# Performance work log

Measured on AMD Instinct MI355X. Metric: run time of the kernel, lower is better.

## Reference

```python
import jax, jax.numpy as jnp
import numpy as np

D_MODEL = 1024  # scaling uses sqrt(d_model), as in the source


def setup_inputs() -> dict:
    key = jax.random.key(0)
    kx, kq, kk, kv = jax.random.split(key, 4)
    B, N, D, H = 4, 4096, D_MODEL, 128
    X = jax.random.normal(kx, (B, N, D), dtype=jnp.float32)
    # nn.Linear(d_model, d_head, bias=False) weights, stored as [d_model, d_head]
    s = 1.0 / np.sqrt(D)
    Wq = jax.random.normal(kq, (D, H), dtype=jnp.float32) * s
    Wk = jax.random.normal(kk, (D, H), dtype=jnp.float32) * s
    Wv = jax.random.normal(kv, (D, H), dtype=jnp.float32) * s
    return {"X": X, "Wq": Wq, "Wk": Wk, "Wv": Wv}


def reference(X, Wq, Wk, Wv):
    # Q, K, V: [B, N, H]
    Q = jnp.einsum("bnd,dh->bnh", X, Wq)
    K = jnp.einsum("bnd,dh->bnh", X, Wk)
    V = jnp.einsum("bnd,dh->bnh", X, Wv)
    # Scores: [B, N, N]; source divides by sqrt(d_model) (not sqrt(d_head))
    A = jnp.einsum("bqh,bkh->bqk", Q, K) / jnp.sqrt(jnp.float32(D_MODEL))
    A = jax.nn.softmax(A, axis=-1)
    # Dropout is identity in eval mode (deterministic reference baseline)
    return jnp.einsum("bqk,bkh->bqh", A, V)
```

## Files before the change

### kernel.cpp

```cpp
#include <hip/hip_runtime.h>
#include <stdint.h>

typedef __bf16 bf16_t;
typedef bf16_t bf16x8 __attribute__((ext_vector_type(8)));
typedef float f32x4 __attribute__((ext_vector_type(4)));
typedef float f32x16 __attribute__((ext_vector_type(16)));
typedef unsigned short u16;
typedef unsigned int u32;

#define MFMA16(a, b, c) __builtin_amdgcn_mfma_f32_16x16x32_bf16((a), (b), (c), 0, 0, 0)
#define MFMA32(a, b, c) __builtin_amdgcn_mfma_f32_32x32x16_bf16((a), (b), (c), 0, 0, 0)

#define QSCALE 0.04508422002778633f

__device__ __forceinline__ u16 f2bf(float f) {
  union { float f; unsigned u; } v; v.f = f;
  unsigned r = v.u + 0x7fffu + ((v.u >> 16) & 1u);
  return (u16)(r >> 16);
}

__device__ __forceinline__ float exp2x(float x) {
#if __has_builtin(__builtin_amdgcn_exp2f)
  return __builtin_amdgcn_exp2f(x);
#else
  return exp2f(x);
#endif
}

__device__ __forceinline__ float rcpx(float x) {
#if __has_builtin(__builtin_amdgcn_rcpf)
  return __builtin_amdgcn_rcpf(x);
#else
  return 1.0f / x;
#endif
}

__device__ __forceinline__ void async_cp16(const void* g, void* l) {
  __builtin_amdgcn_global_load_lds(
      (__attribute__((address_space(1))) void*)(void*)g,
      (__attribute__((address_space(3))) void*)l, 16, 0, 0);
}

__device__ __forceinline__ u32 cvtpk(float lo, float hi) {
  u32 r;
  asm("v_cvt_pk_bf16_f32 %0, %1, %2" : "=v"(r) : "v"(lo), "v"(hi));
  return r;
}
__device__ __forceinline__ void pl32swap(u32& a, u32& b) {
  asm volatile("v_permlane32_swap_b32 %0, %1" : "+v"(a), "+v"(b));
}

__global__ __launch_bounds__(256) void pack_w_k(const float* __restrict__ Wq,
                                                const float* __restrict__ Wk,
                                                const float* __restrict__ Wv,
                                                u16* __restrict__ wp) {
  int t = blockIdx.x * 256 + threadIdx.x;
  int mat = t >> 14;
  int rr = t & 16383;
  int frag = rr >> 6, lane = rr & 63;
  int nt = frag >> 5, kc = frag & 31;
  const float* W = (mat == 0) ? Wq : ((mat == 1) ? Wk : Wv);
  int k0 = kc * 32 + ((lane >> 4) << 3);
  int col = nt * 16 + (lane & 15);
  union { u16 h[8]; uint4 q; } u_;
#pragma unroll
  for (int j = 0; j < 8; ++j) u_.h[j] = f2bf(W[(size_t)(k0 + j) * 128 + col]);
  *(uint4*)(wp + (size_t)t * 8) = u_.q;
}

__device__ __forceinline__ void qkv_stage(const char* Xb, char* dst, int m0,
                                          int kc, int tid) {
#pragma unroll
  for (int i = 0; i < 2; ++i) {
    int p = i * 4096 + tid * 16;
    int row = p >> 8, cb = p & 255;
    int ucb = cb ^ ((row & 7) << 4);
    async_cp16(Xb + ((size_t)(m0 + row) * 4096 + (size_t)kc * 256 + ucb),
               dst + p);
  }
}

__global__ __launch_bounds__(256) void qkv_k(const float* __restrict__ X,
                                             const u16* __restrict__ wp,
                                             u16* __restrict__ Qb,
                                             u16* __restrict__ Kb,
                                             u16* __restrict__ Vt) {
  __shared__ __align__(16) char xs[2][8192];
  const int tid = threadIdx.x;
  const int w = tid >> 6, lane = tid & 63;
  const int r16 = lane >> 4, c16 = lane & 15;
  const int m0 = blockIdx.x * 32;
  const char* Xb = (const char*)X;

  f32x4 acc[2][6];
#pragma unroll
  for (int mt = 0; mt < 2; ++mt)
#pragma unroll
    for (int i = 0; i < 6; ++i) acc[mt][i] = (f32x4){0.f, 0.f, 0.f, 0.f};

  qkv_stage(Xb, xs[0], m0, 0, tid);
  qkv_stage(Xb, xs[1], m0, 1, tid);

  for (int kc = 0; kc < 16; ++kc) {
    if (kc + 1 < 16) {
      asm volatile("s_waitcnt vmcnt(2)" ::: "memory");
    } else {
      asm volatile("s_waitcnt vmcnt(0)" ::: "memory");
    }
    __builtin_amdgcn_s_barrier();
    asm volatile("" ::: "memory");

    const char* xb = xs[kc & 1];
    bf16x8 bw[6][2];
#pragma unroll
    for (int i = 0; i < 6; ++i) {
      int t = w + 4 * i;
      int mat = t >> 3, nt = t & 7;
      const u16* bp = wp + (size_t)mat * 131072 +
                      (size_t)((nt * 32 + kc * 2) * 64 + lane) * 8;
      bw[i][0] = *(const bf16x8*)(bp);
      bw[i][1] = *(const bf16x8*)(bp + 512);
    }
    bf16x8 a[2][2];
#pragma unroll
    for (int mt = 0; mt < 2; ++mt)
#pragma unroll
      for (int ks = 0; ks < 2; ++ks) {
        int row = mt * 16 + c16;
        int swz = (row & 7) << 4;
        int cb0 = ks * 128 + r16 * 32;
        f32x4 lo = *(const f32x4*)(xb + row * 256 + (cb0 ^ swz));
        f32x4 hi = *(const f32x4*)(xb + row * 256 + ((cb0 + 16) ^ swz));
        union { u32 u[4]; bf16x8 v; } pu;
        pu.u[0] = cvtpk(lo[0], lo[1]);
        pu.u[1] = cvtpk(lo[2], lo[3]);
        pu.u[2] = cvtpk(hi[0], hi[1]);
        pu.u[3] = cvtpk(hi[2], hi[3]);
        a[mt][ks] = pu.v;
      }
#pragma unroll
    for (int i = 0; i < 6; ++i)
#pragma unroll
      for (int ks = 0; ks < 2; ++ks)
#pragma unroll
        for (int mt = 0; mt < 2; ++mt)
          acc[mt][i] = MFMA16(a[mt][ks], bw[i][ks], acc[mt][i]);

    asm volatile("" ::: "memory");
    __builtin_amdgcn_s_barrier();
    asm volatile("" ::: "memory");
    if (kc + 2 < 16) qkv_stage(Xb, xs[kc & 1], m0, kc + 2, tid);
  }

  const int batch = m0 >> 12;
#pragma unroll
  for (int i = 0; i < 6; ++i) {
    int t = w + 4 * i;
    int mat = t >> 3, nt = t & 7;
#pragma unroll
    for (int mt = 0; mt < 2; ++mt) {
      f32x4 v = acc[mt][i];
      if (mat == 2) {
        int d = nt * 16 + c16;
        int nloc = (m0 & 4095) + mt * 16 + r16 * 4;
        union { u16 h[4]; uint2 q; } u_;
#pragma unroll
        for (int r = 0; r < 4; ++r) u_.h[r] = f2bf(v[r]);
        *(uint2*)(Vt + ((size_t)(batch * 128 + d)) * 4096 + nloc) = u_.q;
      } else {
        u16* dstm = (mat == 0) ? Qb : Kb;
        float sc = (mat == 0) ? QSCALE : 1.0f;
#pragma unroll
        for (int r = 0; r < 4; ++r) {
          int row = m0 + mt * 16 + r16 * 4 + r;
          dstm[(size_t)row * 128 + nt * 16 + c16] = f2bf(v[r] * sc);
        }
      }
    }
  }
}

__global__ __launch_bounds__(256) void pack_kv_k(const u16* __restrict__ Kb,
                                                 const u16* __restrict__ Vt,
                                                 u16* __restrict__ Kf,
                                                 u16* __restrict__ Vf) {
  int t = blockIdx.x * 256 + threadIdx.x;
  int lane = t & 63, l31 = lane & 31, hi = (lane >> 5) & 1;
  if (t < 262144) {
    int frag = t >> 6;
    int batch = frag >> 10, kt = (frag >> 3) & 127, kc = frag & 7;
    const u16* src = Kb + ((size_t)batch * 4096 + kt * 32 + l31) * 128 + kc * 16 + hi * 8;
    *(uint4*)(Kf + (size_t)t * 8) = *(const uint4*)src;
  } else {
    int o = t - 262144;
    int frag = o >> 6;
    int batch = frag >> 10, tt = (frag >> 4) & 63, ks = (frag >> 2) & 3, dt = frag & 3;
    const u16* src = Vt + ((size_t)batch * 128 + dt * 32 + l31) * 4096 + tt * 64 + ks * 16 + hi * 8;
    *(uint4*)(Vf + (size_t)o * 8) = *(const uint4*)src;
  }
}

__device__ __forceinline__ void stage16(const char* src, char* dst, int tid) {
#pragma unroll
  for (int i = 0; i < 4; ++i)
    async_cp16(src + i * 4096 + tid * 16, dst + i * 4096 + tid * 16);
}

__global__ __launch_bounds__(256, 3) void attn_k(const u16* __restrict__ Qb,
                                                 const u16* __restrict__ Kf,
                                                 const u16* __restrict__ Vf,
                                                 _Float16* __restrict__ Opart,
                                                 float* __restrict__ Ml,
                                                 int nsplit) {
  __shared__ __align__(16) char smem[49152];
  const int tid = threadIdx.x;
  const int w = tid >> 6, lane = tid & 63;
  const int l31 = lane & 31, hi = lane >> 5;

  const int B = gridDim.x;
  int xcd = blockIdx.x & 7, idx = blockIdx.x >> 3;
  int linear = xcd * (B >> 3) + idx;
  int qt = linear & 31, g = linear >> 5;
  int batch = g / nsplit, split = g - batch * nsplit;
  const int q0 = qt * 128;
  const int t0 = (split * 64) / nsplit;
  const int t1 = ((split + 1) * 64) / nsplit;
  const int T = t1 - t0;

  const char* kfc = (const char*)Kf + (size_t)batch * 1048576 + (size_t)t0 * 16384;
  const char* vfc = (const char*)Vf + (size_t)batch * 1048576 + (size_t)t0 * 16384;
  char* vbuf = smem + 32768;

  bf16x8 qf[8];
  const u16* qrow = Qb + ((size_t)batch * 4096 + q0 + w * 32 + l31) * 128 + hi * 8;
#pragma unroll
  for (int kc = 0; kc < 8; ++kc) qf[kc] = *(const bf16x8*)(qrow + kc * 16);

  f32x16 acc[4];
#pragma unroll
  for (int dt = 0; dt < 4; ++dt)
#pragma unroll
    for (int j = 0; j < 16; ++j) acc[dt][j] = 0.f;
  float lacc[8];
#pragma unroll
  for (int i = 0; i < 8; ++i) lacc[i] = 0.f;

  stage16(kfc, smem, tid);
  stage16(vfc, vbuf, tid);
  if (T > 1) stage16(kfc + 16384, smem + 16384, tid);

  for (int t = 0; t < T; ++t) {
    if (t + 1 < T) {
      asm volatile("s_waitcnt vmcnt(8)" ::: "memory");
    } else {
      asm volatile("s_waitcnt vmcnt(4)" ::: "memory");
    }
    __builtin_amdgcn_s_barrier();
    asm volatile("" ::: "memory");
    const char* kb = smem + (t & 1) * 16384;

    f32x16 sv[2];
    __builtin_amdgcn_s_setprio(1);
#pragma unroll
    for (int nt = 0; nt < 2; ++nt) {
      f32x16 s = {};
#pragma unroll
      for (int kc = 0; kc < 8; ++kc) {
        bf16x8 kf = *(const bf16x8*)(kb + (nt * 8 + kc) * 1024 + lane * 16);
        s = MFMA32(kf, qf[kc], s);
      }
      sv[nt] = s;
    }
    __builtin_amdgcn_s_setprio(0);

#pragma unroll
    for (int nt = 0; nt < 2; ++nt)
#pragma unroll
      for (int i = 0; i < 16; ++i) sv[nt][i] = exp2x(sv[nt][i]);
#pragma unroll
    for (int i = 0; i < 8; ++i)
      lacc[i] += (sv[0][i] + sv[0][i + 8]) + (sv[1][i] + sv[1][i + 8]);

    bf16x8 pf[4];
#pragma unroll
    for (int nt = 0; nt < 2; ++nt)
#pragma unroll
      for (int half = 0; half < 2; ++half) {
        const float* p = (const float*)&sv[nt] + half * 8;
        u32 a0 = cvtpk(p[0], p[1]);
        u32 b0 = cvtpk(p[4], p[5]);
        u32 c0 = cvtpk(p[2], p[3]);
        u32 d0 = cvtpk(p[6], p[7]);
        pl32swap(a0, b0);
        pl32swap(c0, d0);
        union { u32 u[4]; bf16x8 v; } pu;
        pu.u[0] = a0; pu.u[1] = c0; pu.u[2] = b0; pu.u[3] = d0;
        pf[nt * 2 + half] = pu.v;
      }

    if (t + 1 < T) {
      asm volatile("s_waitcnt vmcnt(4)" ::: "memory");
    } else {
      asm volatile("s_waitcnt vmcnt(0)" ::: "memory");
    }
    __builtin_amdgcn_s_barrier();
    asm volatile("" ::: "memory");

    __builtin_amdgcn_s_setprio(1);
#pragma unroll
    for (int dt = 0; dt < 4; ++dt) {
#pragma unroll
      for (int ks = 0; ks < 4; ++ks) {
        bf16x8 vf = *(const bf16x8*)(vbuf + (ks * 4 + dt) * 1024 + lane * 16);
        acc[dt] = MFMA32(pf[ks], vf, acc[dt]);
      }
    }
    __builtin_amdgcn_s_setprio(0);

    asm volatile("" ::: "memory");
    __builtin_amdgcn_s_barrier();
    asm volatile("" ::: "memory");

    if (t + 1 < T) stage16(vfc + (size_t)(t + 1) * 16384, vbuf, tid);
    if (t + 2 < T) stage16(kfc + (size_t)(t + 2) * 16384, smem + (t & 1) * 16384, tid);
  }

  float ltot = ((lacc[0] + lacc[1]) + (lacc[2] + lacc[3])) +
               ((lacc[4] + lacc[5]) + (lacc[6] + lacc[7]));
  ltot += __shfl_xor(ltot, 32);

  size_t obase = (size_t)split * 16384 + (size_t)batch * 4096 + q0 + w * 32;
#pragma unroll
  for (int dt = 0; dt < 4; ++dt)
#pragma unroll
    for (int r = 0; r < 16; ++r) {
      int qr = (r & 3) + 8 * (r >> 2) + 4 * hi;
      float lq = __shfl(ltot, qr);
      Opart[(obase + qr) * 128 + dt * 32 + l31] = (_Float16)(acc[dt][r] * rcpx(lq));
    }
  if (lane < 32)
    Ml[(size_t)split * 16384 + (size_t)batch * 4096 + q0 + w * 32 + lane] = ltot;
}

template <int S>
__global__ __launch_bounds__(256) void reduce_k(const _Float16* __restrict__ Op,
                                                const float* __restrict__ Ml,
                                                float* __restrict__ Out) {
  int t = blockIdx.x * 256 + threadIdx.x;
  int q = t >> 4, d8 = (t & 15) << 3;
  float ls[S];
  float L = 0.f;
#pragma unroll
  for (int s = 0; s < S; ++s) {
    ls[s] = Ml[(size_t)s * 16384 + q];
    L += ls[s];
  }
  float o[8] = {0.f, 0.f, 0.f, 0.f, 0.f, 0.f, 0.f, 0.f};
#pragma unroll
  for (int s = 0; s < S; ++s) {
    union { uint4 u; _Float16 h[8]; } pv;
    pv.u = *(const uint4*)(Op + ((size_t)s * 16384 + q) * 128 + d8);
#pragma unroll
    for (int j = 0; j < 8; ++j) o[j] += (float)pv.h[j] * ls[s];
  }
  float inv = rcpx(L);
  float4 r0 = {o[0] * inv, o[1] * inv, o[2] * inv, o[3] * inv};
  float4 r1 = {o[4] * inv, o[5] * inv, o[6] * inv, o[7] * inv};
  *(float4*)(Out + (size_t)q * 128 + d8) = r0;
  *(float4*)(Out + (size_t)q * 128 + d8 + 4) = r1;
}

extern "C" void kernel_launch(void* const* d_in, const int* in_sizes, int n_in,
                              void* d_out, int out_size, void* d_ws, size_t ws_size,
                              hipStream_t stream) {
  const float* X  = (const float*)d_in[0];
  const float* Wq = (const float*)d_in[1];
  const float* Wk = (const float*)d_in[2];
  const float* Wv = (const float*)d_in[3];
  float* Out = (float*)d_out;
  char* ws = (char*)d_ws;
  u16* Qb = (u16*)(ws);
  u16* Kf = (u16*)(ws + (4u << 20));
  u16* Vf = (u16*)(ws + (8u << 20));
  _Float16* Opart = (_Float16*)(ws + (12u << 20));
  u16* Kb = (u16*)(ws + (12u << 20));
  u16* Vt = (u16*)(ws + (16u << 20));
  u16* Wp = (u16*)(ws + (20u << 20));

  int S = (ws_size >= (12ull << 20) + 6ull * (4194304ull + 65536ull)) ? 6 : 4;
  float* Ml = (float*)(ws + (12ull << 20) + (size_t)S * 4194304ull);

  pack_w_k<<<dim3(192), dim3(256), 0, stream>>>(Wq, Wk, Wv, Wp);
  qkv_k<<<dim3(512), dim3(256), 0, stream>>>(X, Wp, Qb, Kb, Vt);
  pack_kv_k<<<dim3(2048), dim3(256), 0, stream>>>(Kb, Vt, Kf, Vf);
  attn_k<<<dim3(128 * S), dim3(256), 0, stream>>>(Qb, Kf, Vf, Opart, Ml, S);
  if (S == 6)
    reduce_k<6><<<dim3(1024), dim3(256), 0, stream>>>(Opart, Ml, Out);
  else
    reduce_k<4><<<dim3(1024), dim3(256), 0, stream>>>(Opart, Ml, Out);
}
```

Baseline: 88.93 us.

## Fuse K/V fragment packing into QKV epilogue and interleave softmax with PV MFMAs

The QKV projection epilogue now stages Q, K and V tiles in swizzled shared memory and writes them straight into the MFMA fragment layouts, so the separate pack_kv_k kernel and its intermediate global round trip go away. Q is also stored in fragment layout so attention loads it with strided fragment reads. Inside the attention loop, the two score tiles are computed separately, and the exp/convert work for the second tile is interleaved with the PV MFMAs of the first, so VALU work can overlap matrix work. The cost is extra shared memory in qkv_k, which may reduce occupancy, and a changed workspace layout.

After: 85.47 us. 3.9% less time.

```diff
diff --git a/kernel.cpp b/kernel.cpp
--- a/kernel.cpp
+++ b/kernel.cpp
@@ -82,13 +82,17 @@
 
 __global__ __launch_bounds__(256) void qkv_k(const float* __restrict__ X,
                                              const u16* __restrict__ wp,
-                                             u16* __restrict__ Qb,
-                                             u16* __restrict__ Kb,
-                                             u16* __restrict__ Vt) {
+                                             u16* __restrict__ Qf,
+                                             u16* __restrict__ Kf,
+                                             u16* __restrict__ Vf) {
   __shared__ __align__(16) char xs[2][8192];
+  __shared__ __align__(16) u16 eq[4096];
+  __shared__ __align__(16) u16 ek[4096];
+  __shared__ __align__(16) u16 ev[4096];
   const int tid = threadIdx.x;
   const int w = tid >> 6, lane = tid & 63;
   const int r16 = lane >> 4, c16 = lane & 15;
+  const int l31 = lane & 31, hi = lane >> 5;
   const int m0 = blockIdx.x * 32;
   const char* Xb = (const char*)X;
 
@@ -130,12 +134,12 @@
         int swz = (row & 7) << 4;
         int cb0 = ks * 128 + r16 * 32;
         f32x4 lo = *(const f32x4*)(xb + row * 256 + (cb0 ^ swz));
-        f32x4 hi = *(const f32x4*)(xb + row * 256 + ((cb0 + 16) ^ swz));
+        f32x4 hi_ = *(const f32x4*)(xb + row * 256 + ((cb0 + 16) ^ swz));
         union { u32 u[4]; bf16x8 v; } pu;
         pu.u[0] = cvtpk(lo[0], lo[1]);
         pu.u[1] = cvtpk(lo[2], lo[3]);
-        pu.u[2] = cvtpk(hi[0], hi[1]);
-        pu.u[3] = cvtpk(hi[2], hi[3]);
+        pu.u[2] = cvtpk(hi_[0], hi_[1]);
+        pu.u[3] = cvtpk(hi_[2], hi_[3]);
         a[mt][ks] = pu.v;
       }
 #pragma unroll
@@ -152,7 +156,6 @@
     if (kc + 2 < 16) qkv_stage(Xb, xs[kc & 1], m0, kc + 2, tid);
   }
 
-  const int batch = m0 >> 12;
 #pragma unroll
   for (int i = 0; i < 6; ++i) {
     int t = w + 4 * i;
@@ -162,41 +165,41 @@
       f32x4 v = acc[mt][i];
       if (mat == 2) {
         int d = nt * 16 + c16;
-        int nloc = (m0 & 4095) + mt * 16 + r16 * 4;
+        int n2 = (mt * 16 + r16 * 4) * 2;
         union { u16 h[4]; uint2 q; } u_;
 #pragma unroll
         for (int r = 0; r < 4; ++r) u_.h[r] = f2bf(v[r]);
-        *(uint2*)(Vt + ((size_t)(batch * 128 + d)) * 4096 + nloc) = u_.q;
+        *(uint2*)((char*)ev + d * 64 + (n2 ^ ((d & 3) << 4))) = u_.q;
       } else {
-        u16* dstm = (mat == 0) ? Qb : Kb;
+        char* tile = (char*)((mat == 0) ? eq : ek);
         float sc = (mat == 0) ? QSCALE : 1.0f;
 #pragma unroll
         for (int r = 0; r < 4; ++r) {
-          int row = m0 + mt * 16 + r16 * 4 + r;
-          dstm[(size_t)row * 128 + nt * 16 + c16] = f2bf(v[r] * sc);
+          int row = mt * 16 + r16 * 4 + r;
+          int cb = (nt * 16 + c16) * 2;
+          *(u16*)(tile + row * 256 + (cb ^ ((row & 15) << 4))) = f2bf(v[r] * sc);
         }
       }
     }
   }
-}
-
-__global__ __launch_bounds__(256) void pack_kv_k(const u16* __restrict__ Kb,
-                                                 const u16* __restrict__ Vt,
-                                                 u16* __restrict__ Kf,
-                                                 u16* __restrict__ Vf) {
-  int t = blockIdx.x * 256 + threadIdx.x;
-  int lane = t & 63, l31 = lane & 31, hi = (lane >> 5) & 1;
-  if (t < 262144) {
-    int frag = t >> 6;
-    int batch = frag >> 10, kt = (frag >> 3) & 127, kc = frag & 7;
-    const u16* src = Kb + ((size_t)batch * 4096 + kt * 32 + l31) * 128 + kc * 16 + hi * 8;
-    *(uint4*)(Kf + (size_t)t * 8) = *(const uint4*)src;
-  } else {
-    int o = t - 262144;
-    int frag = o >> 6;
-    int batch = frag >> 10, tt = (frag >> 4) & 63, ks = (frag >> 2) & 3, dt = frag & 3;
-    const u16* src = Vt + ((size_t)batch * 128 + dt * 32 + l31) * 4096 + tt * 64 + ks * 16 + hi * 8;
-    *(uint4*)(Vf + (size_t)o * 8) = *(const uint4*)src;
+  __syncthreads();
+
+  const int batch = m0 >> 12, loc = m0 & 4095;
+  const int r32 = loc >> 5;
+  const int t64 = loc >> 6, kb0 = (loc & 63) >> 4;
+#pragma unroll
+  for (int p = 0; p < 2; ++p) {
+    int kc = p * 4 + w;
+    int cb = (kc * 16 + hi * 8) * 2;
+    uint4 q_ = *(const uint4*)((const char*)eq + l31 * 256 + (cb ^ ((l31 & 15) << 4)));
+    *(uint4*)(Qf + ((size_t)(batch * 1024 + r32 * 8 + kc) * 64 + lane) * 8) = q_;
+    uint4 k_ = *(const uint4*)((const char*)ek + l31 * 256 + (cb ^ ((l31 & 15) << 4)));
+    *(uint4*)(Kf + ((size_t)(batch * 1024 + r32 * 8 + kc) * 64 + lane) * 8) = k_;
+    int d = w * 32 + l31;
+    uint4 v_ = *(const uint4*)((const char*)ev + d * 64 +
+                               (((p * 16 + hi * 8) * 2) ^ ((d & 3) << 4)));
+    *(uint4*)(Vf + ((size_t)(batch * 1024 + t64 * 16 + (kb0 + p) * 4 + w) * 64 +
+                    lane) * 8) = v_;
   }
 }
 
@@ -206,7 +209,7 @@
     async_cp16(src + i * 4096 + tid * 16, dst + i * 4096 + tid * 16);
 }
 
-__global__ __launch_bounds__(256, 3) void attn_k(const u16* __restrict__ Qb,
+__global__ __launch_bounds__(256, 3) void attn_k(const u16* __restrict__ Qf,
                                                  const u16* __restrict__ Kf,
                                                  const u16* __restrict__ Vf,
                                                  _Float16* __restrict__ Opart,
@@ -232,9 +235,9 @@
   char* vbuf = smem + 32768;
 
   bf16x8 qf[8];
-  const u16* qrow = Qb + ((size_t)batch * 4096 + q0 + w * 32 + l31) * 128 + hi * 8;
-#pragma unroll
-  for (int kc = 0; kc < 8; ++kc) qf[kc] = *(const bf16x8*)(qrow + kc * 16);
+  const u16* qbase = Qf + ((size_t)(batch * 1024 + (qt * 4 + w) * 8) * 64 + lane) * 8;
+#pragma unroll
+  for (int kc = 0; kc < 8; ++kc) qf[kc] = *(const bf16x8*)(qbase + kc * 512);
 
   f32x16 acc[4];
 #pragma unroll
@@ -259,44 +262,40 @@
     asm volatile("" ::: "memory");
     const char* kb = smem + (t & 1) * 16384;
 
-    f32x16 sv[2];
+    f32x16 sv0 = {};
     __builtin_amdgcn_s_setprio(1);
 #pragma unroll
-    for (int nt = 0; nt < 2; ++nt) {
-      f32x16 s = {};
-#pragma unroll
-      for (int kc = 0; kc < 8; ++kc) {
-        bf16x8 kf = *(const bf16x8*)(kb + (nt * 8 + kc) * 1024 + lane * 16);
-        s = MFMA32(kf, qf[kc], s);
-      }
-      sv[nt] = s;
+    for (int kc = 0; kc < 8; ++kc) {
+      bf16x8 kf = *(const bf16x8*)(kb + kc * 1024 + lane * 16);
+      sv0 = MFMA32(kf, qf[kc], sv0);
     }
     __builtin_amdgcn_s_setprio(0);
 
-#pragma unroll
-    for (int nt = 0; nt < 2; ++nt)
-#pragma unroll
-      for (int i = 0; i < 16; ++i) sv[nt][i] = exp2x(sv[nt][i]);
-#pragma unroll
-    for (int i = 0; i < 8; ++i)
-      lacc[i] += (sv[0][i] + sv[0][i + 8]) + (sv[1][i] + sv[1][i + 8]);
+    f32x16 sv1 = {};
+#pragma unroll
+    for (int kc = 0; kc < 8; ++kc) {
+      bf16x8 kf = *(const bf16x8*)(kb + (8 + kc) * 1024 + lane * 16);
+      sv1 = MFMA32(kf, qf[kc], sv1);
+    }
+#pragma unroll
+    for (int i = 0; i < 16; ++i) sv0[i] = exp2x(sv0[i]);
+#pragma unroll
+    for (int i = 0; i < 8; ++i) lacc[i] += sv0[i] + sv0[i + 8];
 
     bf16x8 pf[4];
 #pragma unroll
-    for (int nt = 0; nt < 2; ++nt)
-#pragma unroll
-      for (int half = 0; half < 2; ++half) {
-        const float* p = (const float*)&sv[nt] + half * 8;
-        u32 a0 = cvtpk(p[0], p[1]);
-        u32 b0 = cvtpk(p[4], p[5]);
-        u32 c0 = cvtpk(p[2], p[3]);
-        u32 d0 = cvtpk(p[6], p[7]);
-        pl32swap(a0, b0);
-        pl32swap(c0, d0);
-        union { u32 u[4]; bf16x8 v; } pu;
-        pu.u[0] = a0; pu.u[1] = c0; pu.u[2] = b0; pu.u[3] = d0;
-        pf[nt * 2 + half] = pu.v;
-      }
+    for (int half = 0; half < 2; ++half) {
+      const float* p = (const float*)&sv0 + half * 8;
+      u32 a0 = cvtpk(p[0], p[1]);
+      u32 b0 = cvtpk(p[4], p[5]);
+      u32 c0 = cvtpk(p[2], p[3]);
+      u32 d0 = cvtpk(p[6], p[7]);
+      pl32swap(a0, b0);
+      pl32swap(c0, d0);
+      union { u32 u[4]; bf16x8 v; } pu;
+      pu.u[0] = a0; pu.u[1] = c0; pu.u[2] = b0; pu.u[3] = d0;
+      pf[half] = pu.v;
+    }
 
     if (t + 1 < T) {
       asm volatile("s_waitcnt vmcnt(4)" ::: "memory");
@@ -306,11 +305,37 @@
     __builtin_amdgcn_s_barrier();
     asm volatile("" ::: "memory");
 
+#pragma unroll
+    for (int dt = 0; dt < 4; ++dt) {
+#pragma unroll
+      for (int ks = 0; ks < 2; ++ks) {
+        bf16x8 vf = *(const bf16x8*)(vbuf + (ks * 4 + dt) * 1024 + lane * 16);
+        acc[dt] = MFMA32(pf[ks], vf, acc[dt]);
+      }
+    }
+#pragma unroll
+    for (int i = 0; i < 16; ++i) sv1[i] = exp2x(sv1[i]);
+#pragma unroll
+    for (int i = 0; i < 8; ++i) lacc[i] += sv1[i] + sv1[i + 8];
+#pragma unroll
+    for (int half = 0; half < 2; ++half) {
+      const float* p = (const float*)&sv1 + half * 8;
+      u32 a0 = cvtpk(p[0], p[1]);
+      u32 b0 = cvtpk(p[4], p[5]);
+      u32 c0 = cvtpk(p[2], p[3]);
+      u32 d0 = cvtpk(p[6], p[7]);
+      pl32swap(a0, b0);
+      pl32swap(c0, d0);
+      union { u32 u[4]; bf16x8 v; } pu;
+      pu.u[0] = a0; pu.u[1] = c0; pu.u[2] = b0; pu.u[3] = d0;
+      pf[2 + half] = pu.v;
+    }
+
     __builtin_amdgcn_s_setprio(1);
 #pragma unroll
     for (int dt = 0; dt < 4; ++dt) {
 #pragma unroll
-      for (int ks = 0; ks < 4; ++ks) {
+      for (int ks = 2; ks < 4; ++ks) {
         bf16x8 vf = *(const bf16x8*)(vbuf + (ks * 4 + dt) * 1024 + lane * 16);
         acc[dt] = MFMA32(pf[ks], vf, acc[dt]);
       }
@@ -379,21 +404,18 @@
   const float* Wv = (const float*)d_in[3];
   float* Out = (float*)d_out;
   char* ws = (char*)d_ws;
-  u16* Qb = (u16*)(ws);
+  u16* Qf = (u16*)(ws);
   u16* Kf = (u16*)(ws + (4u << 20));
   u16* Vf = (u16*)(ws + (8u << 20));
-  _Float16* Opart = (_Float16*)(ws + (12u << 20));
-  u16* Kb = (u16*)(ws + (12u << 20));
-  u16* Vt = (u16*)(ws + (16u << 20));
-  u16* Wp = (u16*)(ws + (20u << 20));
-
-  int S = (ws_size >= (12ull << 20) + 6ull * (4194304ull + 65536ull)) ? 6 : 4;
-  float* Ml = (float*)(ws + (12ull << 20) + (size_t)S * 4194304ull);
+  u16* Wp = (u16*)(ws + (12u << 20));
+  _Float16* Opart = (_Float16*)(ws + (13u << 20));
+
+  int S = (ws_size >= (13ull << 20) + 6ull * (4194304ull + 65536ull)) ? 6 : 4;
+  float* Ml = (float*)(ws + (13ull << 20) + (size_t)S * 4194304ull);
 
   pack_w_k<<<dim3(192), dim3(256), 0, stream>>>(Wq, Wk, Wv, Wp);
-  qkv_k<<<dim3(512), dim3(256), 0, stream>>>(X, Wp, Qb, Kb, Vt);
-  pack_kv_k<<<dim3(2048), dim3(256), 0, stream>>>(Kb, Vt, Kf, Vf);
-  attn_k<<<dim3(128 * S), dim3(256), 0, stream>>>(Qb, Kf, Vf, Opart, Ml, S);
+  qkv_k<<<dim3(512), dim3(256), 0, stream>>>(X, Wp, Qf, Kf, Vf);
+  attn_k<<<dim3(128 * S), dim3(256), 0, stream>>>(Qf, Kf, Vf, Opart, Ml, S);
   if (S == 6)
     reduce_k<6><<<dim3(1024), dim3(256), 0, stream>>>(Opart, Ml, Out);
   else
```
